# Kernel optimization log

Measured on AMD Instinct MI355X. Metric: run time of the kernel, lower is better.

The kernel has to match this reference:

```python
import jax, jax.numpy as jnp
import numpy as np

BEAM = 5  # config['beam_size']

def layer_norm(x, g, b, eps=1e-5):
    mu = jnp.mean(x, -1, keepdims=True)
    var = jnp.var(x, -1, keepdims=True)
    return (x - mu) / jnp.sqrt(var + eps) * g + b

def det_topk(logits, mask, k):
    # deterministic (eval-mode) stochastic_topk: masked softmax scores +
    # one-hot select masks for the top-k logits. shapes: logits/mask (M,S)
    ml = jnp.where(mask > 0, logits, -1e9)
    e = jnp.exp(ml - jnp.max(ml, -1, keepdims=True)) * mask
    soft = e / (jnp.sum(e, -1, keepdims=True) + 1e-20)
    _, idx = jax.lax.top_k(ml, k)
    sel = jax.nn.one_hot(idx, logits.shape[-1], dtype=logits.dtype)  # (M,k,S)
    return sel, soft

def grc(l, r, p):
    # Gated Recursive Cell: two-layer MLP -> 4 chunks, softmax gate over
    # {left, right, candidate}, LayerNorm output. l, r: (M, D)
    x = jnp.concatenate([l, r], -1)
    h = jax.nn.gelu(x @ p['Wc1'] + p['bc1'], approximate=False)
    c = (h @ p['Wc2'] + p['bc2']).reshape(l.shape[0], 4, l.shape[-1])
    g = jax.nn.softmax(c[:, 0:3, :], axis=1)
    out = g[:, 0] * l + g[:, 1] * r + g[:, 2] * c[:, 3]
    return layer_norm(out, p['g2'], p['b2'])

def select_composition(content, mask, accu, beam_mask, p):
    N, B, Sp1, D = content.shape
    S = Sp1 - 1
    # decision scores for every adjacent (left, right) pair
    cat = jnp.concatenate([content[:, :, :-1, :], content[:, :, 1:, :]], -1)  # (N,B,S,2D)
    w = (jax.nn.gelu(cat @ p['Wd1'] + p['bd1'], approximate=False) @ p['Wd2'] + p['bd2'])[..., 0]
    topk = min(S, BEAM)
    mNB = jnp.broadcast_to(mask[:, None, :], (N, B, S)).reshape(N * B, S)
    sel, soft = det_topk(w.reshape(N * B, S), mNB, topk)
    soft = soft.reshape(N, B, 1, S)
    sel = sel.reshape(N, B, topk, S)
    new_scores = jnp.log(jnp.sum(sel * soft, -1) + 1e-20)  # (N,B,topk)
    done = (1.0 - mask[:, 0])[:, None, None]
    if topk == 1:
        done_topk = jnp.ones((N, B, 1), content.dtype)
    else:
        done_topk = jnp.concatenate([jnp.ones((N, B, 1), content.dtype),
                                     jnp.zeros((N, B, topk - 1), content.dtype)], -1)
    new_bm = done * done_topk + (1.0 - done)
    beam_mask = (beam_mask[..., None] * new_bm).reshape(N, B * topk)
    accu = (accu[:, :, None] + new_scores).reshape(N, B * topk)
    sel = sel.reshape(N, B * topk, S)
    content = jnp.broadcast_to(content[:, :, None], (N, B, topk, Sp1, D)).reshape(N, B * topk, Sp1, D)
    if B * topk > BEAM:
        # prune expanded beams back to BEAM via one-hot select matmuls
        bsel, _ = det_topk(accu, beam_mask, BEAM)  # (N, BEAM, B*topk)
        content = jnp.einsum('nkb,nbsd->nksd', bsel, content)
        sel = jnp.einsum('nkb,nbs->nks', bsel, sel)
        accu = jnp.einsum('nkb,nb->nk', bsel, accu)
        beam_mask = jnp.einsum('nkb,nb->nk', bsel, beam_mask)
        B2 = BEAM
    else:
        B2 = B * topk
    olc, orc = content[:, :, :-1, :], content[:, :, 1:, :]
    l = jnp.einsum('nbs,nbsd->nbd', sel, olc).reshape(N * B2, D)
    r = jnp.einsum('nbs,nbsd->nbd', sel, orc).reshape(N * B2, D)
    new = grc(l, r, p).reshape(N, B2, 1, D)
    cs = jnp.cumsum(sel, -1)
    # splice merged node back: left of merge keeps olc, right keeps orc
    new = sel[..., None] * new + (1.0 - cs)[..., None] * olc + (cs - sel)[..., None] * orc
    return content, new, accu, beam_mask

def _forward(x, mask, p):
    N, S, _ = x.shape
    content = layer_norm(x @ p['Wi'] + p['bi'], p['g1'], p['b1'])[:, None]  # (N,1,S,D)
    D = content.shape[-1]
    accu = jnp.zeros((N, 1), x.dtype)
    beam_mask = jnp.ones((N, 1), x.dtype)
    for i in range(S - 1):
        B = content.shape[1]
        if i < S - 2:
            old, new, accu, beam_mask = select_composition(content, mask[:, i + 1:], accu, beam_mask, p)
        else:
            old = content  # (N,B,2,D)
            l = content[:, :, 0, :].reshape(N * B, D)
            r = content[:, :, 1, :].reshape(N * B, D)
            new = grc(l, r, p).reshape(N, B, 1, D)
        done = mask[:, i + 1][:, None, None, None]
        content = done * new + (1.0 - done) * old[:, :, :-1, :]
    h = content[:, :, 0, :]  # (N,B,D)
    scores = beam_mask * accu + (1.0 - beam_mask) * (-999999.0)
    w = jax.nn.softmax(scores, -1)
    return jnp.sum(w[..., None] * h, axis=1)  # global_state (N,D)

def setup_inputs() -> dict:
    key = jax.random.key(0)
    ks = jax.random.split(key, 6)
    N, S, WD, D = 256, 32, 512, 512
    CH = 4 * D
    def lin(k, fi, fo):
        return (jax.random.normal(k, (fi, fo), jnp.float32) / np.sqrt(fi).astype(np.float32))
    return {
        'x': jax.random.normal(ks[0], (N, S, WD), jnp.float32),
        'mask': jnp.ones((N, S), jnp.float32),
        'Wi': lin(ks[1], WD, D), 'bi': jnp.zeros((D,), jnp.float32),
        'g1': jnp.ones((D,), jnp.float32), 'b1': jnp.zeros((D,), jnp.float32),
        'Wd1': lin(ks[2], 2 * D, D), 'bd1': jnp.zeros((D,), jnp.float32),
        'Wd2': lin(ks[3], D, 1), 'bd2': jnp.zeros((1,), jnp.float32),
        'Wc1': lin(ks[4], 2 * D, CH), 'bc1': jnp.zeros((CH,), jnp.float32),
        'Wc2': lin(ks[5], CH, 4 * D), 'bc2': jnp.zeros((4 * D,), jnp.float32),
        'g2': jnp.ones((D,), jnp.float32), 'b2': jnp.zeros((D,), jnp.float32),
    }

def reference(x, mask, Wi, bi, g1, b1, Wd1, bd1, Wd2, bd2, Wc1, bc1, Wc2, bc2, g2, b2):
    p = dict(Wi=Wi, bi=bi, g1=g1, b1=b1, Wd1=Wd1, bd1=bd1, Wd2=Wd2, bd2=bd2,
             Wc1=Wc1, bc1=bc1, Wc2=Wc2, bc2=bc2, g2=g2, b2=b2)
    return _forward(x, mask, p)
```

## Files before the change

### kernel.cpp

```cpp
#include <hip/hip_runtime.h>
#include <math.h>


#define NN   256
#define S0   32
#define WDIM 512
#define DD   512
#define CHID 2048
#define BEAM 5
#define NB   (NN*BEAM)
#define RSCALE 2048.0f
#define RINV  (1.0f/2048.0f)
#define AR_INIT 8192
#define AR_TOT  (AR_INIT + 30*NB)
#define MN2 ((size_t)NB*CHID)

typedef __attribute__((ext_vector_type(8))) _Float16 f16x8;
typedef __attribute__((ext_vector_type(4))) float f32x4;

__device__ __forceinline__ float gelu_f(float x) {
    return 0.5f * x * (1.0f + erff(x * 0.7071067811865475f));
}
__device__ __forceinline__ _Float16 hi16(float v) { return (_Float16)v; }
__device__ __forceinline__ _Float16 lo16(float v, _Float16 h) {
    return (_Float16)((v - (float)h) * RSCALE);
}
__device__ __forceinline__ float recon(_Float16 h, _Float16 l) {
    return (float)h + RINV * (float)l;
}

__device__ __forceinline__ void gload_lds16(const void* g, void* l) {
    __builtin_amdgcn_global_load_lds(
        (const __attribute__((address_space(1))) unsigned*)g,
        (__attribute__((address_space(3))) unsigned*)l, 16, 0, 0);
}

__device__ __forceinline__ float block_reduce_sum(float v, float* sb) {
    #pragma unroll
    for (int o = 32; o > 0; o >>= 1) v += __shfl_down(v, o);
    const int lane = threadIdx.x & 63, wid = threadIdx.x >> 6;
    __syncthreads();
    if (lane == 0) sb[wid] = v;
    __syncthreads();
    return sb[0] + sb[1] + sb[2] + sb[3];
}

template<int AIDX>
__global__ __launch_bounds__(256, 1) void k_gemm(
    const _Float16* __restrict__ Ah, const _Float16* __restrict__ Al,
    const _Float16* __restrict__ Bh, const _Float16* __restrict__ Bl,
    const float* __restrict__ bias, float* __restrict__ Cf,
    int M, int N, int Ktot, int Kchunk)
{
    __shared__ __align__(16) _Float16 lds[2][4 * 4096];
    const int t = threadIdx.x, wave = t >> 6, lane = t & 63;
    const int bm = blockIdx.y * 128, bn = blockIdx.x * 128;
    const int koff = blockIdx.z * Kchunk;
    const int wm = (wave >> 1) * 64, wn = (wave & 1) * 64;
    const int rsub = lane >> 2, seg = lane & 3;
    const int fm = lane & 15, fko = (lane >> 4) * 8;

    f32x4 acc0[4][4], acc1[4][4];
    #pragma unroll
    for (int i = 0; i < 4; ++i)
        #pragma unroll
        for (int j = 0; j < 4; ++j) {
            acc0[i][j] = (f32x4){0.f, 0.f, 0.f, 0.f};
            acc1[i][j] = (f32x4){0.f, 0.f, 0.f, 0.f};
        }

    const int iters = Kchunk >> 5;
    #define STAGE_G(IT, BUF) {                                                 \
        const int k = koff + (IT)*32;                                          \
        _Float16* Lb = &lds[BUF][0];                                           \
        _Pragma("unroll")                                                      \
        for (int j = 0; j < 2; ++j) {                                          \
            const int q = wave * 2 + j;                                        \
            const size_t aoff = (size_t)(bm + q*16 + rsub) * Ktot + k + seg*8; \
            const size_t boff = (size_t)(bn + q*16 + rsub) * Ktot + k + seg*8; \
            gload_lds16(Ah + aoff, Lb + 0*4096 + q*512);                       \
            gload_lds16(Al + aoff, Lb + 1*4096 + q*512);                       \
            gload_lds16(Bh + boff, Lb + 2*4096 + q*512);                       \
            gload_lds16(Bl + boff, Lb + 3*4096 + q*512);                       \
        } }

    STAGE_G(0, 0);
    for (int it = 0; it < iters; ++it) {
        __syncthreads();
        if (it + 1 < iters) STAGE_G(it + 1, (it + 1) & 1);
        const _Float16* L = &lds[it & 1][0];
        f16x8 ah[4], al[4];
        #pragma unroll
        for (int i = 0; i < 4; ++i) {
            const int ar = wm + i*16 + fm;
            ah[i] = *(const f16x8*)&L[0*4096 + ar*32 + fko];
            al[i] = *(const f16x8*)&L[1*4096 + ar*32 + fko];
        }
        #pragma unroll
        for (int j = 0; j < 4; ++j) {
            const int br = wn + j*16 + fm;
            f16x8 bh = *(const f16x8*)&L[2*4096 + br*32 + fko];
            f16x8 bl = *(const f16x8*)&L[3*4096 + br*32 + fko];
            #pragma unroll
            for (int i = 0; i < 4; ++i) {
                acc0[i][j] = __builtin_amdgcn_mfma_f32_16x16x32_f16(ah[i], bh, acc0[i][j], 0, 0, 0);
                acc1[i][j] = __builtin_amdgcn_mfma_f32_16x16x32_f16(ah[i], bl, acc1[i][j], 0, 0, 0);
                acc1[i][j] = __builtin_amdgcn_mfma_f32_16x16x32_f16(al[i], bh, acc1[i][j], 0, 0, 0);
            }
        }
    }
    float* dst = Cf + (size_t)blockIdx.z * M * N;
    #pragma unroll
    for (int i = 0; i < 4; ++i)
        #pragma unroll
        for (int j = 0; j < 4; ++j) {
            const int col = bn + wn + j*16 + fm;
            const float bv = (blockIdx.z == 0) ? bias[col] : 0.f;
            #pragma unroll
            for (int r = 0; r < 4; ++r) {
                const int row = bm + wm + i*16 + (lane >> 4)*4 + r;
                dst[(size_t)row * N + col] = acc0[i][j][r] + acc1[i][j][r] * RINV + bv;
            }
        }
    #undef STAGE_G
}

template<int AIDX>
__global__ __launch_bounds__(256, 1) void k_gemm1(
    const _Float16* __restrict__ Ah, const _Float16* __restrict__ Al,
    const _Float16* __restrict__ Bh, const _Float16* __restrict__ Bl,
    const float* __restrict__ bias,
    _Float16* __restrict__ Oh, _Float16* __restrict__ Ol,
    const int* __restrict__ lrid, const int* __restrict__ rrid,
    const int* __restrict__ idxt, int N)
{
    __shared__ __align__(16) _Float16 lds[2][12288];
    const int t = threadIdx.x, wave = t >> 6, lane = t & 63;
    const int bm = blockIdx.y * 128, bn = blockIdx.x * 64;
    const int rsub = lane >> 2, seg = lane & 3;
    const int fm = lane & 15, quad = lane >> 4, fko = quad * 8;

    size_t lb[2], rb[2];
    #pragma unroll
    for (int j = 0; j < 2; ++j) {
        const int rowm = bm + (wave*2 + j)*16 + rsub;
        if (AIDX == 1) {
            lb[j] = (size_t)lrid[rowm] * 512;
            rb[j] = (size_t)rrid[rowm] * 512;
        } else {
            lb[j] = (size_t)idxt[rowm*31 + 0] * 512;
            rb[j] = (size_t)idxt[rowm*31 + 1] * 512;
        }
    }
    const size_t bbase = (size_t)(bn + wave*16 + rsub) * 1024;

    f32x4 acc0[2][4], acc1[2][4];
    #pragma unroll
    for (int i = 0; i < 2; ++i)
        #pragma unroll
        for (int j = 0; j < 4; ++j) {
            acc0[i][j] = (f32x4){0.f, 0.f, 0.f, 0.f};
            acc1[i][j] = (f32x4){0.f, 0.f, 0.f, 0.f};
        }

    #define STAGE_G1(IT, BUF) {                                                 \
        const int k0 = (IT)*32;                                                 \
        _Float16* Lb = &lds[BUF][0];                                            \
        _Pragma("unroll")                                                       \
        for (int j = 0; j < 2; ++j) {                                           \
            const int q = wave*2 + j;                                           \
            const size_t aoff = (k0 < 512 ? lb[j] + k0 : rb[j] + (k0-512)) + seg*8; \
            gload_lds16(Ah + aoff, Lb + q*512);                                 \
            gload_lds16(Al + aoff, Lb + 4096 + q*512);                          \
        }                                                                       \
        gload_lds16(Bh + bbase + k0 + seg*8, Lb + 8192 + wave*512);             \
        gload_lds16(Bl + bbase + k0 + seg*8, Lb + 10240 + wave*512); }

    STAGE_G1(0, 0);
    for (int it = 0; it < 32; ++it) {
        __syncthreads();
        if (it + 1 < 32) STAGE_G1(it + 1, (it + 1) & 1);
        const _Float16* L = &lds[it & 1][0];
        f16x8 ah[2], al[2];
        #pragma unroll
        for (int i = 0; i < 2; ++i) {
            const int ar = wave*32 + i*16 + fm;
            ah[i] = *(const f16x8*)&L[ar*32 + fko];
            al[i] = *(const f16x8*)&L[4096 + ar*32 + fko];
        }
        #pragma unroll
        for (int j = 0; j < 4; ++j) {
            const int br = j*16 + fm;
            f16x8 bh = *(const f16x8*)&L[8192 + br*32 + fko];
            f16x8 bl = *(const f16x8*)&L[10240 + br*32 + fko];
            #pragma unroll
            for (int i = 0; i < 2; ++i) {
                acc0[i][j] = __builtin_amdgcn_mfma_f32_16x16x32_f16(ah[i], bh, acc0[i][j], 0, 0, 0);
                acc1[i][j] = __builtin_amdgcn_mfma_f32_16x16x32_f16(ah[i], bl, acc1[i][j], 0, 0, 0);
                acc1[i][j] = __builtin_amdgcn_mfma_f32_16x16x32_f16(al[i], bh, acc1[i][j], 0, 0, 0);
            }
        }
    }
    #pragma unroll
    for (int i = 0; i < 2; ++i)
        #pragma unroll
        for (int j = 0; j < 4; ++j) {
            const int col = bn + j*16 + fm;
            const float bv = bias[col];
            #pragma unroll
            for (int r = 0; r < 4; ++r) {
                const int row = bm + wave*32 + i*16 + quad*4 + r;
                float v = gelu_f(acc0[i][j][r] + acc1[i][j][r] * RINV + bv);
                _Float16 h = hi16(v);
                Oh[(size_t)row * N + col] = h;
                Ol[(size_t)row * N + col] = lo16(v, h);
            }
        }
    #undef STAGE_G1
}

template<int MODE>
__global__ __launch_bounds__(256, 2) void k_wscore(
    const _Float16* __restrict__ ch, const _Float16* __restrict__ cl,
    const int* __restrict__ posb, const int* __restrict__ idxt,
    const _Float16* __restrict__ Bh, const _Float16* __restrict__ Bl,
    const float* __restrict__ bd1, const float* __restrict__ u512,
    const float* __restrict__ bd2, float* __restrict__ w, int Spairs)
{
    __shared__ __align__(16) _Float16 lds[2][8192];
    const int t = threadIdx.x, wave = t >> 6, lane = t & 63;
    const int bm = blockIdx.x * 64, ncol0 = blockIdx.y * 64;
    const int rsub = lane >> 2, seg = lane & 3;
    const int fm = lane & 15, quad = lane >> 4, fko = quad * 8;

    size_t lb, rb;
    {
        const int rowm = bm + wave*16 + rsub;
        int lrow, rrow;
        if (MODE == 0) {
            const int n = rowm / 31, s = rowm - n * 31;
            lrow = n*32 + s; rrow = lrow + 1;
        } else {
            const int nk = rowm >> 1, slot = rowm & 1;
            const int s = posb[nk];
            int jw = s - 1 + slot;
            int jc = jw < 0 ? 0 : (jw > Spairs - 1 ? Spairs - 1 : jw);
            lrow = idxt[nk*31 + jc]; rrow = idxt[nk*31 + jc + 1];
        }
        lb = (size_t)lrow * 512; rb = (size_t)rrow * 512;
    }
    const size_t bbase = (size_t)(ncol0 + wave*16 + rsub) * 1024;

    f32x4 acc0[4], acc1[4];
    #pragma unroll
    for (int j = 0; j < 4; ++j) {
        acc0[j] = (f32x4){0.f, 0.f, 0.f, 0.f};
        acc1[j] = (f32x4){0.f, 0.f, 0.f, 0.f};
    }
    #define STAGE_WS(IT, BUF) {                                                \
        const int k0 = (IT)*32;                                                \
        _Float16* Lb = &lds[BUF][0];                                           \
        const size_t aoff = (k0 < 512 ? lb + k0 : rb + (k0-512)) + seg*8;      \
        gload_lds16(ch + aoff, Lb + 0*2048 + wave*512);                        \
        gload_lds16(cl + aoff, Lb + 1*2048 + wave*512);                        \
        gload_lds16(Bh + bbase + k0 + seg*8, Lb + 2*2048 + wave*512);          \
        gload_lds16(Bl + bbase + k0 + seg*8, Lb + 3*2048 + wave*512); }

    STAGE_WS(0, 0);
    for (int it = 0; it < 32; ++it) {
        __syncthreads();
        if (it + 1 < 32) STAGE_WS(it + 1, (it + 1) & 1);
        const _Float16* L = &lds[it & 1][0];
        const int ar = wave*16 + fm;
        f16x8 ah = *(const f16x8*)&L[0*2048 + ar*32 + fko];
        f16x8 al = *(const f16x8*)&L[1*2048 + ar*32 + fko];
        #pragma unroll
        for (int j = 0; j < 4; ++j) {
            const int br = j*16 + fm;
            f16x8 bh = *(const f16x8*)&L[2*2048 + br*32 + fko];
            f16x8 bl = *(const f16x8*)&L[3*2048 + br*32 + fko];
            acc0[j] = __builtin_amdgcn_mfma_f32_16x16x32_f16(ah, bh, acc0[j], 0, 0, 0);
            acc1[j] = __builtin_amdgcn_mfma_f32_16x16x32_f16(ah, bl, acc1[j], 0, 0, 0);
            acc1[j] = __builtin_amdgcn_mfma_f32_16x16x32_f16(al, bh, acc1[j], 0, 0, 0);
        }
    }
    float part[4] = {0.f, 0.f, 0.f, 0.f};
    #pragma unroll
    for (int j = 0; j < 4; ++j) {
        const int col = ncol0 + j*16 + fm;
        const float bv = bd1[col], uv = u512[col];
        #pragma unroll
        for (int r = 0; r < 4; ++r) {
            float v = acc0[j][r] + acc1[j][r] * RINV + bv;
            part[r] += gelu_f(v) * uv;
        }
    }
    #pragma unroll
    for (int r = 0; r < 4; ++r) {
        float s = part[r];
        s += __shfl_xor(s, 1); s += __shfl_xor(s, 2);
        s += __shfl_xor(s, 4); s += __shfl_xor(s, 8);
        part[r] = s;
    }
    if (fm == 0) {
        const float bd2v = (blockIdx.y == 0) ? bd2[0] : 0.f;
        #pragma unroll
        for (int r = 0; r < 4; ++r) {
            const int rowm = bm + wave*16 + quad*4 + r;
            int wi = -1;
            if (MODE == 0) {
                const int n = rowm / 31, s = rowm - n * 31;
                wi = n * BEAM * S0 + s;
            } else {
                const int nk = rowm >> 1, slot = rowm & 1;
                const int jw = posb[nk] - 1 + slot;
                if (jw >= 0 && jw < Spairs) wi = nk * S0 + jw;
            }
            if (wi >= 0) atomicAdd(&w[wi], part[r] + bd2v);
        }
    }
    #undef STAGE_WS
}

__global__ __launch_bounds__(256) void k_tsplit(
    const float* __restrict__ in, _Float16* __restrict__ oh,
    _Float16* __restrict__ ol, int K, int N)
{
    __shared__ float tile[32][33];
    const int bx = blockIdx.x * 32, by = blockIdx.y * 32;
    const int t = threadIdx.x, r = t >> 5, c = t & 31;
    #pragma unroll
    for (int p = 0; p < 4; ++p)
        tile[r + p*8][c] = in[(size_t)(by + r + p*8) * N + bx + c];
    __syncthreads();
    #pragma unroll
    for (int p = 0; p < 4; ++p) {
        const int nl = r + p*8;
        float v = tile[c][nl];
        _Float16 h = hi16(v);
        oh[(size_t)(bx + nl) * K + by + c] = h;
        ol[(size_t)(bx + nl) * K + by + c] = lo16(v, h);
    }
}

__global__ __launch_bounds__(256) void k_xsplit(
    const float* __restrict__ in, _Float16* __restrict__ oh,
    _Float16* __restrict__ ol)
{
    const size_t i = ((size_t)blockIdx.x * 256 + threadIdx.x) * 4;
    float4 v = *(const float4*)(in + i);
    _Float16 h0 = hi16(v.x), h1 = hi16(v.y), h2 = hi16(v.z), h3 = hi16(v.w);
    typedef __attribute__((ext_vector_type(4))) _Float16 f16x4v;
    f16x4v h = {h0, h1, h2, h3};
    f16x4v l = {lo16(v.x,h0), lo16(v.y,h1), lo16(v.z,h2), lo16(v.w,h3)};
    *(f16x4v*)(oh + i) = h;
    *(f16x4v*)(ol + i) = l;
}

__global__ __launch_bounds__(256) void k_ln_init(
    const float* __restrict__ y, const float* __restrict__ g,
    const float* __restrict__ b, _Float16* __restrict__ cha,
    _Float16* __restrict__ cla)
{
    const int row = blockIdx.x;
    const float* yr = y + (size_t)row * DD;
    const int t = threadIdx.x;
    float v0 = yr[t], v1 = yr[t + 256];
    __shared__ float sb[8];
    float s1 = block_reduce_sum(v0 + v1, sb);
    float s2 = block_reduce_sum(v0*v0 + v1*v1, sb);
    float mu = s1 * (1.f/512.f);
    float rstd = rsqrtf(s2 * (1.f/512.f) - mu*mu + 1e-5f);
    float a0 = (v0 - mu) * rstd * g[t]       + b[t];
    float a1 = (v1 - mu) * rstd * g[t + 256] + b[t + 256];
    _Float16 h0 = hi16(a0), h1 = hi16(a1);
    cha[(size_t)row*DD + t]       = h0;
    cla[(size_t)row*DD + t]       = lo16(a0, h0);
    cha[(size_t)row*DD + t + 256] = h1;
    cla[(size_t)row*DD + t + 256] = lo16(a1, h1);
}

__global__ void k_init_state(float* accu, float* bm, int* idx0, float* wz) {
    int i = blockIdx.x * blockDim.x + threadIdx.x;
    if (i < NB*S0) wz[i] = 0.f;
    if (i < AR_INIT) idx0[i] = i;
    if (i < NB) { accu[i] = 0.f; bm[i] = 1.f; }
}

__global__ __launch_bounds__(320) void k_topk(
    const float* __restrict__ w, const float* __restrict__ accu,
    const float* __restrict__ bmask, const float* __restrict__ maskg,
    int iiter, int B, int S, int topk, int do_bsel,
    const int* __restrict__ idxold, int BAo, int STo,
    int* __restrict__ parent, int* __restrict__ posb,
    int* __restrict__ lrid, int* __restrict__ rrid,
    float* __restrict__ accu_out, float* __restrict__ bm_out,
    float* __restrict__ wnew, int Snew, int dow)
{
    const int n = blockIdx.x, t = threadIdx.x;
    const int wave = t >> 6, lane = t & 63;
    __shared__ int   selpos_s[BEAM][BEAM];
    __shared__ float nscore_s[BEAM][BEAM];
    __shared__ int   par_s[BEAM], pos_s[BEAM];
    const float* mrow = maskg + n*S0 + (iiter + 1);
    const float mk   = (lane < S) ? mrow[lane] : 0.f;
    const float done = 1.f - mrow[0];
    if (wave < B) {
        const int b = wave;
        float ml;
        if (lane < S) {
            float wv = w[(n*BEAM + b)*S0 + lane];
            ml = (mk > 0.f) ? wv : -1e9f;
        } else ml = -INFINITY;
        float mx = ml;
        #pragma unroll
        for (int o = 32; o > 0; o >>= 1) mx = fmaxf(mx, __shfl_xor(mx, o));
        float e = (lane < S) ? expf(ml - mx) * mk : 0.f;
        float es = e;
        #pragma unroll
        for (int o = 32; o > 0; o >>= 1) es += __shfl_xor(es, o);
        const float den = es + 1e-20f;
        float mlc = ml;
        for (int ts = 0; ts < topk; ++ts) {
            unsigned int fb = __float_as_uint(mlc);
            unsigned int ok = (fb & 0x80000000u) ? ~fb : (fb | 0x80000000u);
            unsigned long long key =
                ((unsigned long long)ok << 32) | (unsigned int)(63 - lane);
            if (lane >= S) key = 0ull;
            unsigned long long km = key;
            #pragma unroll
            for (int o = 32; o > 0; o >>= 1) {
                unsigned long long oth = __shfl_xor(km, o);
                km = (oth > km) ? oth : km;
            }
            int sidx = 63 - (int)(km & 0xffffffffull);
            float esel = __shfl(e, sidx);
            if (lane == 0) {
                selpos_s[b][ts] = sidx;
                nscore_s[b][ts] = logf(esel / den + 1e-20f);
            }
            if (lane == sidx) mlc = -INFINITY;
        }
    }
    __syncthreads();
    if (wave == 0) {
        const int C = B * topk;
        float ac = 0.f, bc = 0.f;
        if (lane < C) {
            const int pb = lane / topk, ptt = lane - pb * topk;
            ac = accu[n*BEAM + pb] + nscore_s[pb][ptt];
            const float nb = done * ((ptt == 0) ? 1.f : 0.f) + (1.f - done);
            bc = bmask[n*BEAM + pb] * nb;
        }
        bool used = false;
        for (int k = 0; k < BEAM; ++k) {
            int bestc;
            if (do_bsel) {
                const float v = (lane < C && !used)
                                ? ((bc > 0.f) ? ac : -1e9f) : -INFINITY;
                unsigned fb = __float_as_uint(v);
                unsigned ok = (fb & 0x80000000u) ? ~fb : (fb | 0x80000000u);
                unsigned long long key =
                    ((unsigned long long)ok << 32) | (unsigned)(63 - lane);
                unsigned long long km = key;
                #pragma unroll
                for (int o = 32; o > 0; o >>= 1) {
                    unsigned long long oth = __shfl_xor(km, o);
                    km = (oth > km) ? oth : km;
                }
                bestc = 63 - (int)(km & 0xffffffffull);
            } else bestc = k;
            if (lane == bestc) used = true;
            const float av  = __shfl(ac, bestc);
            const float bv2 = __shfl(bc, bestc);
            const int pp = bestc / topk, ss = selpos_s[pp][bestc - pp * topk];
            if (lane == 0) {
                parent[n*BEAM + k] = pp;
                posb[n*BEAM + k]   = ss;
                par_s[k] = pp; pos_s[k] = ss;
                accu_out[n*BEAM + k] = av;
                bm_out[n*BEAM + k]   = bv2;
            }
        }
    }
    __syncthreads();
    if (t < BEAM) {
        const int base = (n*BAo + par_s[t]) * STo + pos_s[t];
        lrid[n*BEAM + t] = idxold[base];
        rrid[n*BEAM + t] = idxold[base + 1];
    }
    if (dow && wave < BEAM) {
        const int k = wave;
        const int p = par_s[k], s = pos_s[k];
        if (lane < Snew) {
            float v = 0.f;
            if (lane < s - 1)      v = w[(n*BEAM + p)*S0 + lane];
            else if (lane > s)     v = w[(n*BEAM + p)*S0 + lane + 1];
            wnew[(n*BEAM + k)*S0 + lane] = v;
        }
    }
}

__global__ __launch_bounds__(256) void k_compose(
    const float* __restrict__ P,
    const _Float16* __restrict__ cha_r, const _Float16* __restrict__ cla_r,
    const int* __restrict__ lrid, const int* __restrict__ rrid,
    const int* __restrict__ parent, const int* __restrict__ posb,
    const int* __restrict__ idxold, int BAo, int STo,
    const float* __restrict__ maskg, int iiter, int Spnew,
    const float* __restrict__ gp, const float* __restrict__ bp,
    _Float16* __restrict__ cha_w, _Float16* __restrict__ cla_w, int newbase,
    int* __restrict__ idxnew, int finalflag, float* __restrict__ nvout)
{
    __shared__ float sb[8];
    const int nk = blockIdx.x, t = threadIdx.x;
    const int n = nk / BEAM;
    size_t lbase, rbase;
    if (finalflag) {
        lbase = (size_t)idxold[nk*31 + 0] * 512;
        rbase = (size_t)idxold[nk*31 + 1] * 512;
    } else {
        lbase = (size_t)lrid[nk] * 512;
        rbase = (size_t)rrid[nk] * 512;
    }
    const float* c = P + (size_t)nk * CHID;
    float o[2];
    #pragma unroll
    for (int e = 0; e < 2; ++e) {
        const int d = t + 256*e;
        const float lv = recon(cha_r[lbase + d], cla_r[lbase + d]);
        const float rv = recon(cha_r[rbase + d], cla_r[rbase + d]);
        float c0 = ((c[d]        + c[MN2 + d])        + c[2*MN2 + d])        + c[3*MN2 + d];
        float c1 = ((c[DD + d]   + c[MN2 + DD + d])   + c[2*MN2 + DD + d])   + c[3*MN2 + DD + d];
        float c2 = ((c[2*DD + d] + c[MN2 + 2*DD + d]) + c[2*MN2 + 2*DD + d]) + c[3*MN2 + 2*DD + d];
        float c3 = ((c[3*DD + d] + c[MN2 + 3*DD + d]) + c[2*MN2 + 3*DD + d]) + c[3*MN2 + 3*DD + d];
        float m = fmaxf(c0, fmaxf(c1, c2));
        float e0 = expf(c0 - m), e1 = expf(c1 - m), e2 = expf(c2 - m);
        float inv = 1.f / (e0 + e1 + e2);
        o[e] = (e0*lv + e1*rv + e2*c3) * inv;
    }
    float s1 = block_reduce_sum(o[0] + o[1], sb);
    float s2 = block_reduce_sum(o[0]*o[0] + o[1]*o[1], sb);
    float mu = s1 * (1.f/512.f);
    float rstd = rsqrtf(s2 * (1.f/512.f) - mu*mu + 1e-5f);
    if (finalflag) {
        #pragma unroll
        for (int e = 0; e < 2; ++e) {
            const int d = t + 256*e;
            nvout[(size_t)nk*DD + d] = (o[e] - mu) * rstd * gp[d] + bp[d];
        }
        return;
    }
    const int arow = newbase + nk;
    #pragma unroll
    for (int e = 0; e < 2; ++e) {
        const int d = t + 256*e;
        float v = (o[e] - mu) * rstd * gp[d] + bp[d];
        _Float16 h = hi16(v);
        cha_w[(size_t)arow*512 + d] = h;
        cla_w[(size_t)arow*512 + d] = lo16(v, h);
    }
    if (t < Spnew) {
        const float done = maskg[n*S0 + iiter + 1];
        const int p = parent[nk], s = posb[nk];
        const int src = (n*BAo + p) * STo;
        int val;
        if (done > 0.5f)
            val = (t < s) ? idxold[src + t] : (t == s ? arow : idxold[src + t + 1]);
        else
            val = idxold[src + t];
        idxnew[nk*31 + t] = val;
    }
}

__global__ __launch_bounds__(256) void k_final(
    const float* __restrict__ nv,
    const _Float16* __restrict__ cha, const _Float16* __restrict__ cla,
    const int* __restrict__ idxt, const float* __restrict__ maskg,
    const float* __restrict__ accu, const float* __restrict__ bmv,
    float* __restrict__ out)
{
    const int n = blockIdx.x, t = threadIdx.x;
    const float done = maskg[n*S0 + 31];
    float sc[BEAM];
    #pragma unroll
    for (int k = 0; k < BEAM; ++k) {
        float m = bmv[n*BEAM + k];
        sc[k] = m * accu[n*BEAM + k] + (1.f - m) * (-999999.f);
    }
    float mx = sc[0];
    #pragma unroll
    for (int k = 1; k < BEAM; ++k) mx = fmaxf(mx, sc[k]);
    float e[BEAM], den = 0.f;
    #pragma unroll
    for (int k = 0; k < BEAM; ++k) { e[k] = expf(sc[k] - mx); den += e[k]; }
    const float inv = 1.f / den;
    #pragma unroll
    for (int i2 = 0; i2 < 2; ++i2) {
        const int d = t + 256*i2;
        float s = 0.f;
        #pragma unroll
        for (int k = 0; k < BEAM; ++k) {
            const int nk = n*BEAM + k;
            const size_t ob = (size_t)idxt[nk*31] * 512;
            const float nvv  = nv[(size_t)nk*DD + d];
            const float oldv = recon(cha[ob + d], cla[ob + d]);
            s += e[k]*inv * (done*nvv + (1.f - done)*oldv);
        }
        out[(size_t)n*DD + d] = s;
    }
}

extern "C" void kernel_launch(void* const* d_in, const int* in_sizes, int n_in,
                              void* d_out, int out_size, void* d_ws, size_t ws_size,
                              hipStream_t stream) {
    (void)in_sizes; (void)n_in; (void)out_size; (void)ws_size;
    const float* x    = (const float*)d_in[0];
    const float* mask = (const float*)d_in[1];
    const float* Wi   = (const float*)d_in[2];
    const float* bi   = (const float*)d_in[3];
    const float* g1   = (const float*)d_in[4];
    const float* b1   = (const float*)d_in[5];
    const float* Wd1  = (const float*)d_in[6];
    const float* bd1  = (const float*)d_in[7];
    const float* Wd2  = (const float*)d_in[8];
    const float* bd2  = (const float*)d_in[9];
    const float* Wc1  = (const float*)d_in[10];
    const float* bc1  = (const float*)d_in[11];
    const float* Wc2  = (const float*)d_in[12];
    const float* bc2  = (const float*)d_in[13];
    const float* g2   = (const float*)d_in[14];
    const float* b2   = (const float*)d_in[15];
    float* out = (float*)d_out;

    char* p = (char*)d_ws;
    _Float16* cha = (_Float16*)p;        p += (size_t)AR_TOT*512*2;
    _Float16* cla = (_Float16*)p;        p += (size_t)AR_TOT*512*2;
    _Float16* Wc1th = (_Float16*)p;      p += (size_t)CHID*1024*2;
    _Float16* Wc1tl = (_Float16*)p;      p += (size_t)CHID*1024*2;
    _Float16* Wc2th = (_Float16*)p;      p += (size_t)CHID*CHID*2;
    _Float16* Wc2tl = (_Float16*)p;      p += (size_t)CHID*CHID*2;
    _Float16* Wd1th = (_Float16*)p;      p += (size_t)512*1024*2;
    _Float16* Wd1tl = (_Float16*)p;      p += (size_t)512*1024*2;
    _Float16* Wih = (_Float16*)p;        p += (size_t)WDIM*DD*2;
    _Float16* Wil = (_Float16*)p;        p += (size_t)WDIM*DD*2;
    _Float16* Hh  = (_Float16*)p;        p += (size_t)NB*CHID*2;
    _Float16* Hl  = (_Float16*)p;        p += (size_t)NB*CHID*2;
    float* Pb   = (float*)p;             p += MN2*4*4;
    float* nvb  = (float*)p;             p += (size_t)NB*DD*4;
    float* wA   = (float*)p;             p += (size_t)NB*S0*4;
    float* wB   = (float*)p;             p += (size_t)NB*S0*4;
    float* accA = (float*)p;             p += NB*4;
    float* accB = (float*)p;             p += NB*4;
    float* bmA  = (float*)p;             p += NB*4;
    float* bmB  = (float*)p;             p += NB*4;
    int* parent = (int*)p;               p += NB*4;
    int* posb   = (int*)p;               p += NB*4;
    int* lrid   = (int*)p;               p += NB*4;
    int* rrid   = (int*)p;               p += NB*4;
    int* idx0   = (int*)p;               p += AR_INIT*4;
    int* idxA   = (int*)p;               p += NB*31*4;
    int* idxB   = (int*)p;               p += NB*31*4;
    _Float16* xh = (_Float16*)Pb;
    _Float16* xl = (_Float16*)((char*)Pb + (size_t)AR_INIT*512*2);
    float* ybuf  = (float*)((char*)Pb + (size_t)AR_INIT*512*4);

    k_tsplit<<<dim3(CHID/32, 1024/32), 256, 0, stream>>>(Wc1, Wc1th, Wc1tl, 1024, CHID);
    k_tsplit<<<dim3(CHID/32, CHID/32), 256, 0, stream>>>(Wc2, Wc2th, Wc2tl, CHID, CHID);
    k_tsplit<<<dim3(512/32, 1024/32), 256, 0, stream>>>(Wd1, Wd1th, Wd1tl, 1024, 512);
    k_tsplit<<<dim3(DD/32, WDIM/32), 256, 0, stream>>>(Wi, Wih, Wil, WDIM, DD);
    k_init_state<<<(NB*S0 + 255)/256, 256, 0, stream>>>(accA, bmA, idx0, wA);

    k_xsplit<<<(AR_INIT*WDIM)/1024, 256, 0, stream>>>(x, xh, xl);
    k_gemm<0><<<dim3(DD/128, AR_INIT/128, 1), 256, 0, stream>>>(
        xh, xl, Wih, Wil, bi, ybuf, AR_INIT, DD, WDIM, WDIM);
    k_ln_init<<<AR_INIT, 256, 0, stream>>>(ybuf, g1, b1, cha, cla);
    k_wscore<0><<<dim3(NN*31/64, 8), 256, 0, stream>>>(
        cha, cla, nullptr, nullptr, Wd1th, Wd1tl, bd1, Wd2, bd2, wA, 31);

    const int* idxcur = idx0;
    int* idxnxt = idxA;
    int BAo = 1, STo = 32;
    float *wcur = wA, *wnxt = wB;
    float *acur = accA, *anxt = accB, *bcur = bmA, *bnxt = bmB;
    for (int i = 0; i < 30; ++i) {
        const int B  = (i == 0) ? 1 : BEAM;
        const int S  = 31 - i;
        const int tk = (S < BEAM) ? S : BEAM;
        const int dob = (B*tk > BEAM) ? 1 : 0;
        const int newbase = AR_INIT + i*NB;
        k_topk<<<NN, 320, 0, stream>>>(wcur, acur, bcur, mask, i, B, S, tk, dob,
                                       idxcur, BAo, STo, parent, posb, lrid, rrid,
                                       anxt, bnxt, wnxt, S - 1, (i < 29) ? 1 : 0);
        k_gemm1<1><<<dim3(CHID/64, NB/128), 256, 0, stream>>>(
            cha, cla, Wc1th, Wc1tl, bc1, Hh, Hl, lrid, rrid, nullptr, CHID);
        k_gemm<0><<<dim3(CHID/128, NB/128, 4), 256, 0, stream>>>(
            Hh, Hl, Wc2th, Wc2tl, bc2, Pb, NB, CHID, CHID, 512);
        k_compose<<<NB, 256, 0, stream>>>(Pb, cha, cla, lrid, rrid, parent, posb,
                                          idxcur, BAo, STo, mask, i, 31 - i,
                                          g2, b2, cha, cla, newbase, idxnxt,
                                          0, nullptr);
        if (i < 29)
            k_wscore<1><<<dim3(NB*2/64, 8), 256, 0, stream>>>(
                cha, cla, posb, idxnxt, Wd1th, Wd1tl, bd1, Wd2, bd2, wnxt, S - 1);
        idxcur = idxnxt;
        idxnxt = (idxnxt == idxA) ? idxB : idxA;
        BAo = BEAM; STo = 31;
        float* tp;
        tp = wcur; wcur = wnxt; wnxt = tp;
        tp = acur; acur = anxt; anxt = tp;
        tp = bcur; bcur = bnxt; bnxt = tp;
    }
    k_gemm1<2><<<dim3(CHID/64, NB/128), 256, 0, stream>>>(
        cha, cla, Wc1th, Wc1tl, bc1, Hh, Hl, nullptr, nullptr, idxcur, CHID);
    k_gemm<0><<<dim3(CHID/128, NB/128, 4), 256, 0, stream>>>(
        Hh, Hl, Wc2th, Wc2tl, bc2, Pb, NB, CHID, CHID, 512);
    k_compose<<<NB, 256, 0, stream>>>(Pb, cha, cla, nullptr, nullptr, parent, posb,
                                      idxcur, BEAM, 31, mask, 30, 0,
                                      g2, b2, nullptr, nullptr, 0,
                                      nullptr, 1, nvb);
    k_final<<<NN, 256, 0, stream>>>(nvb, cha, cla, idxcur, mask, acur, bcur, out);
}
```

Baseline: 4.105 ms.

## Deepen LDS prefetch pipelines with explicit vmcnt waits in GEMM kernels

Replaces double-buffered LDS staging with a 4-stage ring in k_gemm and 3-stage rings in k_gemm1 and k_wscore. __syncthreads is replaced by partial s_waitcnt vmcnt waits plus a raw s_barrier, so more global-to-LDS loads stay in flight while MFMA work runs. This is meant to hide global memory latency, at the cost of more LDS per block (k_gemm goes to 128KB). Correctness depends on the vmcnt counts matching the number of loads issued per stage.

```diff
diff --git a/kernel.cpp b/kernel.cpp
--- a/kernel.cpp
+++ b/kernel.cpp
@@ -35,6 +35,14 @@
         (__attribute__((address_space(3))) unsigned*)l, 16, 0, 0);
 }
 
+__device__ __forceinline__ void barrier_mem() {
+    asm volatile("s_barrier" ::: "memory");
+}
+template<int N>
+__device__ __forceinline__ void wait_vmcnt() {
+    asm volatile("s_waitcnt vmcnt(%0)" :: "i"(N) : "memory");
+}
+
 __device__ __forceinline__ float block_reduce_sum(float v, float* sb) {
     #pragma unroll
     for (int o = 32; o > 0; o >>= 1) v += __shfl_down(v, o);
@@ -52,7 +60,7 @@
     const float* __restrict__ bias, float* __restrict__ Cf,
     int M, int N, int Ktot, int Kchunk)
 {
-    __shared__ __align__(16) _Float16 lds[2][4 * 4096];
+    __shared__ __align__(16) _Float16 lds[4][4 * 4096];
     const int t = threadIdx.x, wave = t >> 6, lane = t & 63;
     const int bm = blockIdx.y * 128, bn = blockIdx.x * 128;
     const int koff = blockIdx.z * Kchunk;
@@ -85,10 +93,16 @@
         } }
 
     STAGE_G(0, 0);
+    if (1 < iters) STAGE_G(1, 1);
+    if (2 < iters) STAGE_G(2, 2);
     for (int it = 0; it < iters; ++it) {
-        __syncthreads();
-        if (it + 1 < iters) STAGE_G(it + 1, (it + 1) & 1);
-        const _Float16* L = &lds[it & 1][0];
+        const int rem = iters - it;
+        if (rem > 2)      wait_vmcnt<16>();
+        else if (rem == 2) wait_vmcnt<8>();
+        else              wait_vmcnt<0>();
+        barrier_mem();
+        if (it + 3 < iters) STAGE_G(it + 3, (it + 3) & 3);
+        const _Float16* L = &lds[it & 3][0];
         f16x8 ah[4], al[4];
         #pragma unroll
         for (int i = 0; i < 4; ++i) {
@@ -134,7 +148,7 @@
     const int* __restrict__ lrid, const int* __restrict__ rrid,
     const int* __restrict__ idxt, int N)
 {
-    __shared__ __align__(16) _Float16 lds[2][12288];
+    __shared__ __align__(16) _Float16 lds[3][12288];
     const int t = threadIdx.x, wave = t >> 6, lane = t & 63;
     const int bm = blockIdx.y * 128, bn = blockIdx.x * 64;
     const int rsub = lane >> 2, seg = lane & 3;
@@ -177,10 +191,13 @@
         gload_lds16(Bl + bbase + k0 + seg*8, Lb + 10240 + wave*512); }
 
     STAGE_G1(0, 0);
+    STAGE_G1(1, 1);
     for (int it = 0; it < 32; ++it) {
-        __syncthreads();
-        if (it + 1 < 32) STAGE_G1(it + 1, (it + 1) & 1);
-        const _Float16* L = &lds[it & 1][0];
+        if (it < 31) wait_vmcnt<6>();
+        else         wait_vmcnt<0>();
+        barrier_mem();
+        if (it + 2 < 32) STAGE_G1(it + 2, (it + 2) % 3);
+        const _Float16* L = &lds[it % 3][0];
         f16x8 ah[2], al[2];
         #pragma unroll
         for (int i = 0; i < 2; ++i) {
@@ -227,7 +244,7 @@
     const float* __restrict__ bd1, const float* __restrict__ u512,
     const float* __restrict__ bd2, float* __restrict__ w, int Spairs)
 {
-    __shared__ __align__(16) _Float16 lds[2][8192];
+    __shared__ __align__(16) _Float16 lds[3][8192];
     const int t = threadIdx.x, wave = t >> 6, lane = t & 63;
     const int bm = blockIdx.x * 64, ncol0 = blockIdx.y * 64;
     const int rsub = lane >> 2, seg = lane & 3;
@@ -267,10 +284,13 @@
         gload_lds16(Bl + bbase + k0 + seg*8, Lb + 3*2048 + wave*512); }
 
     STAGE_WS(0, 0);
+    STAGE_WS(1, 1);
     for (int it = 0; it < 32; ++it) {
-        __syncthreads();
-        if (it + 1 < 32) STAGE_WS(it + 1, (it + 1) & 1);
-        const _Float16* L = &lds[it & 1][0];
+        if (it < 31) wait_vmcnt<4>();
+        else         wait_vmcnt<0>();
+        barrier_mem();
+        if (it + 2 < 32) STAGE_WS(it + 2, (it + 2) % 3);
+        const _Float16* L = &lds[it % 3][0];
         const int ar = wave*16 + fm;
         f16x8 ah = *(const f16x8*)&L[0*2048 + ar*32 + fko];
         f16x8 al = *(const f16x8*)&L[1*2048 + ar*32 + fko];
```

Measured after the change: 4.163 ms. Within noise of the previous version (+1.4%).
